# Kernel tuning notes

Measured on AMD Instinct MI355X. Metric: run time of the kernel, lower is better.

## Reference

```python
import jax, jax.numpy as jnp
import numpy as np
from jax import lax

EPS = 1e-06


def _ema_scan(x, s):
    # x: [B, C, T]; s: [C] smoothing coeff in [0, 1]
    # Recurrence: y_0 = x_0; y_t = s * x_t + (1 - s) * y_{t-1}
    # Expressed as affine pairs (A_t, b_t) with y_t = A_t * y_{t-1} + b_t
    s_b = s[None, :, None]  # [1, C, 1]
    A0 = jnp.zeros_like(x[:, :, :1])
    A_rest = jnp.broadcast_to(1.0 - s_b, x[:, :, 1:].shape)
    A = jnp.concatenate([A0, A_rest], axis=2)
    b = jnp.concatenate([x[:, :, :1], s_b * x[:, :, 1:]], axis=2)

    def combine(c1, c2):
        a1, b1 = c1
        a2, b2 = c2
        return (a1 * a2, a2 * b1 + b2)

    _, ema = lax.associative_scan(combine, (A, b), axis=2)
    return ema


def setup_inputs() -> dict:
    key = jax.random.key(0)
    B, C, T = 32, 128, 16000
    kx, = jax.random.split(key, 1)
    x = jax.random.uniform(kx, (B, C, T), dtype=jnp.float32)
    alpha = jnp.ones((C,), dtype=jnp.float32) * 0.96
    delta = jnp.ones((C,), dtype=jnp.float32) * 2.0
    root = jnp.ones((C,), dtype=jnp.float32) * 2.0
    ema_weights = jnp.ones((C,), dtype=jnp.float32) * 0.04
    return {"x": x, "alpha": alpha, "delta": delta, "root": root, "ema_weights": ema_weights}


def reference(x, alpha, delta, root, ema_weights):
    # sPCEN: per-channel EMA smoother + power-law compression
    s = jnp.clip(ema_weights, 0.0, 1.0)
    ema = _ema_scan(x, s)  # [B, C, T]

    alpha_c = jnp.minimum(alpha, 1.0)[None, :, None]
    root_c = jnp.maximum(root, 1.0)[None, :, None]
    r = 1.0 / root_c
    d = delta[None, :, None]

    out = (x / (EPS + ema) ** alpha_c + d) ** r - d ** r
    return out
```

## Files before the change

kernel.cpp:

```cpp
#include <hip/hip_runtime.h>
#include <math.h>

#define T_LEN    16000
#define T_LEN4   4000
#define THREADS  256
#define CHUNK    16
#define TILE4    (THREADS * 4)
#define NT       4
#define EPS_F    1e-6f

__launch_bounds__(THREADS, 6)
__global__ void pcen_kernel(const float* __restrict__ x,
                            const float* __restrict__ alpha,
                            const float* __restrict__ delta,
                            const float* __restrict__ root,
                            const float* __restrict__ ema_w,
                            float* __restrict__ out, int C) {
    __shared__ float swA[2][4], swB[2][4];

    const int row  = blockIdx.x;
    const int c    = row % C;
    const int tid  = threadIdx.x;
    const int lane = tid & 63;
    const int wave = tid >> 6;

    const float s   = fminf(fmaxf(ema_w[c], 0.0f), 1.0f);
    const float q   = 1.0f - s;
    const float a_c = fminf(alpha[c], 1.0f);
    const float r   = 1.0f / fmaxf(root[c], 1.0f);
    const float d   = delta[c];
    const float dr  = powf(d, r);
    const float q16 = powf(q, (float)CHUNK);
    const bool  sqrt_path = (r == 0.5f);

    const float4* x4 = (const float4*)(x   + (size_t)row * T_LEN);
    float4*       o4 = (float4*)      (out + (size_t)row * T_LEN);

    float e_carry = 0.0f;

    for (int t = 0; t < NT; ++t) {
        const int  base4 = t * TILE4 + tid * 4;
        const bool valid = (base4 < T_LEN4);
        const int  p     = t & 1;

        float4 v0, v1, v2, v3;
        if (valid) {
            v0 = x4[base4 + 0]; v1 = x4[base4 + 1];
            v2 = x4[base4 + 2]; v3 = x4[base4 + 3];
        } else {
            v0 = v1 = v2 = v3 = make_float4(1.f, 1.f, 1.f, 1.f);
        }
        float xv[CHUNK] = { v0.x, v0.y, v0.z, v0.w,  v1.x, v1.y, v1.z, v1.w,
                            v2.x, v2.y, v2.z, v2.w,  v3.x, v3.y, v3.z, v3.w };

        const bool ft = (t == 0) && (tid == 0);
        float la = ft ? 0.0f  : q16;
        float lb = ft ? xv[0] : s * xv[0];
        #pragma unroll
        for (int j = 1; j < CHUNK; ++j) lb = fmaf(q, lb, s * xv[j]);

        #pragma unroll
        for (int off = 1; off < 64; off <<= 1) {
            float ua = __shfl_up(la, off);
            float ub = __shfl_up(lb, off);
            if (lane >= off) { lb = fmaf(la, ub, lb); la *= ua; }
        }
        if (lane == 63) { swA[p][wave] = la; swB[p][wave] = lb; }
        __syncthreads();

        float pa = 1.0f, pb = 0.0f;
        #pragma unroll
        for (int w = 0; w < 3; ++w)
            if (w < wave) { pb = fmaf(swA[p][w], pb, swB[p][w]); pa *= swA[p][w]; }

        float ea = __shfl_up(la, 1);
        float eb = __shfl_up(lb, 1);
        float a_ex, b_ex;
        if (lane == 0) { a_ex = pa;      b_ex = pb; }
        else           { a_ex = pa * ea; b_ex = fmaf(ea, pb, eb); }
        float e = fmaf(a_ex, e_carry, b_ex);

        float ta = 1.0f, tb = 0.0f;
        #pragma unroll
        for (int w = 0; w < 4; ++w) { tb = fmaf(swA[p][w], tb, swB[p][w]); ta *= swA[p][w]; }
        e_carry = fmaf(ta, e_carry, tb);

        if (valid) {
            if (sqrt_path) {
                #pragma unroll
                for (int j = 0; j < CHUNK; ++j) {
                    float xvj = xv[j];
                    e = (ft && j == 0) ? xvj : fmaf(q, e, s * xvj);
                    float lge = log2f(EPS_F + e);
                    float v   = xvj * exp2f(-a_c * lge);
                    xv[j] = sqrtf(v + d) - dr;
                }
            } else {
                #pragma unroll
                for (int j = 0; j < CHUNK; ++j) {
                    float xvj = xv[j];
                    e = (ft && j == 0) ? xvj : fmaf(q, e, s * xvj);
                    float lge = log2f(EPS_F + e);
                    float v   = xvj * exp2f(-a_c * lge);
                    xv[j] = exp2f(r * log2f(v + d)) - dr;
                }
            }
            o4[base4 + 0] = make_float4(xv[ 0], xv[ 1], xv[ 2], xv[ 3]);
            o4[base4 + 1] = make_float4(xv[ 4], xv[ 5], xv[ 6], xv[ 7]);
            o4[base4 + 2] = make_float4(xv[ 8], xv[ 9], xv[10], xv[11]);
            o4[base4 + 3] = make_float4(xv[12], xv[13], xv[14], xv[15]);
        }
    }
}

extern "C" void kernel_launch(void* const* d_in, const int* in_sizes, int n_in,
                              void* d_out, int out_size, void* d_ws, size_t ws_size,
                              hipStream_t stream) {
    const float* x     = (const float*)d_in[0];
    const float* alpha = (const float*)d_in[1];
    const float* delta = (const float*)d_in[2];
    const float* root  = (const float*)d_in[3];
    const float* ema_w = (const float*)d_in[4];
    float* out = (float*)d_out;

    const int C    = in_sizes[1];
    const int rows = in_sizes[0] / T_LEN;

    pcen_kernel<<<rows, THREADS, 0, stream>>>(x, alpha, delta, root, ema_w, out, C);
}
```

Measured before the change: 456.0 us.

## Prefetch next tile into registers and replace syncthreads with raw barrier

Each tile's global loads are now issued one iteration ahead into a second set of float4 registers, so memory latency can overlap the scan and transcendental work of the current tile. The __syncthreads is replaced by an explicit lgkmcnt wait plus s_barrier, so the barrier no longer waits on outstanding vector memory (the prefetch). Occupancy bound is lowered from 6 to 5 to make room for the extra registers, which trades fewer resident waves for per-wave latency hiding.

```diff
diff --git a/kernel.cpp b/kernel.cpp
--- a/kernel.cpp
+++ b/kernel.cpp
@@ -9,7 +9,7 @@
 #define NT       4
 #define EPS_F    1e-6f
 
-__launch_bounds__(THREADS, 6)
+__launch_bounds__(THREADS, 5)
 __global__ void pcen_kernel(const float* __restrict__ x,
                             const float* __restrict__ alpha,
                             const float* __restrict__ delta,
@@ -38,20 +38,22 @@
 
     float e_carry = 0.0f;
 
-    for (int t = 0; t < NT; ++t) {
+    auto loadt = [&](int t, float4& r0, float4& r1, float4& r2, float4& r3) {
+        const int b = t * TILE4 + tid * 4;
+        if (b < T_LEN4) { r0 = x4[b]; r1 = x4[b+1]; r2 = x4[b+2]; r3 = x4[b+3]; }
+        else            { r0 = r1 = r2 = r3 = make_float4(1.f, 1.f, 1.f, 1.f); }
+    };
+
+    auto body = [&](int t, float4& c0, float4& c1, float4& c2, float4& c3,
+                    bool pref, float4& n0, float4& n1, float4& n2, float4& n3) {
         const int  base4 = t * TILE4 + tid * 4;
         const bool valid = (base4 < T_LEN4);
         const int  p     = t & 1;
 
-        float4 v0, v1, v2, v3;
-        if (valid) {
-            v0 = x4[base4 + 0]; v1 = x4[base4 + 1];
-            v2 = x4[base4 + 2]; v3 = x4[base4 + 3];
-        } else {
-            v0 = v1 = v2 = v3 = make_float4(1.f, 1.f, 1.f, 1.f);
-        }
-        float xv[CHUNK] = { v0.x, v0.y, v0.z, v0.w,  v1.x, v1.y, v1.z, v1.w,
-                            v2.x, v2.y, v2.z, v2.w,  v3.x, v3.y, v3.z, v3.w };
+        float xv[CHUNK] = { c0.x, c0.y, c0.z, c0.w,  c1.x, c1.y, c1.z, c1.w,
+                            c2.x, c2.y, c2.z, c2.w,  c3.x, c3.y, c3.z, c3.w };
+
+        if (pref) loadt(t + 1, n0, n1, n2, n3);
 
         const bool ft = (t == 0) && (tid == 0);
         float la = ft ? 0.0f  : q16;
@@ -66,7 +68,9 @@
             if (lane >= off) { lb = fmaf(la, ub, lb); la *= ua; }
         }
         if (lane == 63) { swA[p][wave] = la; swB[p][wave] = lb; }
-        __syncthreads();
+
+        asm volatile("s_waitcnt lgkmcnt(0)" ::: "memory");
+        __builtin_amdgcn_s_barrier();
 
         float pa = 1.0f, pb = 0.0f;
         #pragma unroll
@@ -110,7 +114,14 @@
             o4[base4 + 2] = make_float4(xv[ 8], xv[ 9], xv[10], xv[11]);
             o4[base4 + 3] = make_float4(xv[12], xv[13], xv[14], xv[15]);
         }
-    }
+    };
+
+    float4 a0, a1, a2, a3, b0, b1, b2, b3;
+    loadt(0, a0, a1, a2, a3);
+    body(0, a0, a1, a2, a3, true,  b0, b1, b2, b3);
+    body(1, b0, b1, b2, b3, true,  a0, a1, a2, a3);
+    body(2, a0, a1, a2, a3, true,  b0, b1, b2, b3);
+    body(3, b0, b1, b2, b3, false, a0, a1, a2, a3);
 }
 
 extern "C" void kernel_launch(void* const* d_in, const int* in_sizes, int n_in,
```

Result: no change. 449.1 us (-1.5%).
